# Optimization experiments

Hardware: AMD Instinct MI355X
Metric: run time of the kernel (lower is better)

Reference implementation:

```python
import jax, jax.numpy as jnp
import numpy as np

B, N, C, H = 8, 1024, 768, 12
HEAD_DIM = C // H
EPS = 1e-6


def setup_inputs() -> dict:
    key = jax.random.key(0)
    k1, k2, k3, k4, k5 = jax.random.split(key, 5)
    x = jax.random.normal(k1, (B, N, C), dtype=jnp.float32)
    # binary keep-mask per token, shape (B, N, 1)
    policy = (jax.random.uniform(k2, (B, N, 1)) > 0.3).astype(jnp.float32)
    Wqkv = jax.random.normal(k3, (3 * C, C), dtype=jnp.float32) * 0.02
    Wproj = jax.random.normal(k4, (C, C), dtype=jnp.float32) * 0.02
    bproj = jax.random.normal(k5, (C,), dtype=jnp.float32) * 0.02
    return {"x": x, "policy": policy, "Wqkv": Wqkv, "Wproj": Wproj, "bproj": bproj}


def softmax_with_policy(attn, policy, eps=EPS):
    # attn: (B,H,N,N), policy: (B,N,1) in {0,1}
    Bb, _, Nn, _ = attn.shape
    ap1 = policy.reshape(Bb, 1, 1, Nn)          # key mask
    ap2 = policy.reshape(Bb, 1, Nn, 1)          # query mask
    eye = jnp.eye(Nn, dtype=policy.dtype)[None, None]
    attn_policy = ap1 * ap2 + (1.0 - ap1) * eye  # (B,1,N,N)
    max_att = jnp.max(attn, axis=-1, keepdims=True)
    a = jnp.exp(attn - max_att).astype(jnp.float32) * attn_policy.astype(jnp.float32)
    a = (a + eps / Nn) / (jnp.sum(a, axis=-1, keepdims=True) + eps)
    return a.astype(attn.dtype)


def reference(x, policy, Wqkv, Wproj, bproj):
    Bb, Nn, Cc = x.shape
    scale = HEAD_DIM ** -0.5
    qkv = (x @ Wqkv.T).reshape(Bb, Nn, 3, H, HEAD_DIM).transpose(2, 0, 3, 1, 4)
    q, k, v = qkv[0], qkv[1], qkv[2]            # each (B,H,N,hd)
    attn = jnp.einsum('bhnd,bhmd->bhnm', q, k) * scale
    attn = softmax_with_policy(attn, policy)
    out = jnp.einsum('bhnm,bhmd->bhnd', attn, v)  # (B,H,N,hd)
    out = out.transpose(0, 2, 1, 3).reshape(Bb, Nn, Cc)
    return out @ Wproj.T + bproj
```

## Files before the change

kernel.cpp:

```cpp
#include <hip/hip_runtime.h>
#include <hip/hip_bf16.h>
#include <stdint.h>

#define Bdim 8
#define Nseq 1024
#define Cdim 768
#define Hn 12
#define HD 64
#define EPSf 1e-6f

typedef __bf16 bf16;
typedef __bf16 bf16x8 __attribute__((ext_vector_type(8)));
typedef float f32x4 __attribute__((ext_vector_type(4)));

static __device__ __forceinline__ void gload_lds16(const bf16* g, bf16* lds) {
  __builtin_amdgcn_global_load_lds(
      (const __attribute__((address_space(1))) uint32_t*)g,
      (__attribute__((address_space(3))) uint32_t*)lds, 16, 0, 0);
}

#define NX (Bdim * Nseq * Cdim)
#define NWQ (3 * Cdim * Cdim)
#define NWP (Cdim * Cdim)
__global__ __launch_bounds__(256) void cvt_all(
    const float* __restrict__ x, const float* __restrict__ wq, const float* __restrict__ wp,
    bf16* __restrict__ Xb, bf16* __restrict__ Wqb, bf16* __restrict__ Wpb,
    float* __restrict__ CS) {
  if (blockIdx.x < 24) CS[blockIdx.x * 256 + threadIdx.x] = 0.f;
  const int i = (blockIdx.x * 256 + threadIdx.x) * 8;
  const float* src;
  bf16* dst;
  int off;
  if (i < NX) { src = x; dst = Xb; off = i; }
  else if (i < NX + NWQ) { src = wq; dst = Wqb; off = i - NX; }
  else { src = wp; dst = Wpb; off = i - NX - NWQ; }
  float4 a = *(const float4*)(src + off);
  float4 b = *(const float4*)(src + off + 4);
  bf16x8 o;
  o[0] = (bf16)a.x; o[1] = (bf16)a.y; o[2] = (bf16)a.z; o[3] = (bf16)a.w;
  o[4] = (bf16)b.x; o[5] = (bf16)b.y; o[6] = (bf16)b.z; o[7] = (bf16)b.w;
  *(bf16x8*)(dst + off) = o;
}

__global__ __launch_bounds__(256) void gemm_qkv(
    const bf16* __restrict__ X, const bf16* __restrict__ W,
    bf16* __restrict__ Qb, bf16* __restrict__ Kb, bf16* __restrict__ Vt,
    float* __restrict__ CS) {
  __shared__ __align__(16) bf16 As[128 * 64];
  __shared__ __align__(16) bf16 Bs[128 * 64];
  const int t = threadIdx.x;
  const int lane = t & 63;
  const int w = t >> 6;
  const int l15 = lane & 15, quad = lane >> 4;
  const int wm = w & 1, wn = w >> 1;
  constexpr int K = Cdim;

  const int flat = blockIdx.y * 18 + blockIdx.x;
  const int xcd = flat & 7, idx = flat >> 3;
  const int my = (idx & 7) + xcd * 8;
  const int nx = idx >> 3;
  const int mbase = my * 128;
  const int nbase = nx * 128;

  const int srow = t >> 3, slot = t & 7;
  f32x4 acc[4][4] = {};

  for (int kt = 0; kt < K; kt += 64) {
#pragma unroll
    for (int j = 0; j < 4; j++) {
      const int row = j * 32 + srow;
      const int seg = slot ^ (row & 7);
      gload_lds16(X + (size_t)(mbase + row) * K + kt + seg * 8, As + (j * 256 + t) * 8);
    }
#pragma unroll
    for (int j = 0; j < 4; j++) {
      const int row = j * 32 + srow;
      const int seg = slot ^ (row & 7);
      gload_lds16(W + (size_t)(nbase + row) * K + kt + seg * 8, Bs + (j * 256 + t) * 8);
    }
    __syncthreads();
#pragma unroll
    for (int kh = 0; kh < 2; kh++) {
      bf16x8 a[4], b[4];
#pragma unroll
      for (int mt = 0; mt < 4; mt++) {
        const int row = wm * 64 + mt * 16 + l15;
        a[mt] = *(const bf16x8*)(As + row * 64 + ((kh * 4 + quad) ^ (row & 7)) * 8);
      }
#pragma unroll
      for (int nt = 0; nt < 4; nt++) {
        const int row = wn * 64 + nt * 16 + l15;
        b[nt] = *(const bf16x8*)(Bs + row * 64 + ((kh * 4 + quad) ^ (row & 7)) * 8);
      }
#pragma unroll
      for (int mt = 0; mt < 4; mt++)
#pragma unroll
        for (int nt = 0; nt < 4; nt++)
          acc[mt][nt] = __builtin_amdgcn_mfma_f32_16x16x32_bf16(a[mt], b[nt], acc[mt][nt], 0, 0, 0);
    }
    __syncthreads();
  }

  const int s = nbase / Cdim;
  const float oscale = (s == 0) ? 0.125f : 1.0f;
  const int jbase = (nbase % Cdim) + wn * 64;
  const int b0 = mbase >> 10;
#pragma unroll
  for (int nt = 0; nt < 4; nt++) {
    const int jj = jbase + nt * 16 + l15;
    const int h = jj >> 6, d = jj & 63;
#pragma unroll
    for (int mt = 0; mt < 4; mt++) {
#pragma unroll
      for (int r = 0; r < 4; r++) {
        const int m = mbase + wm * 64 + mt * 16 + quad * 4 + r;
        const int n = m & 1023;
        const bf16 v = (bf16)(acc[mt][nt][r] * oscale);
        const size_t bh = (size_t)b0 * Hn + h;
        if (s == 0)      Qb[(bh * Nseq + n) * HD + d] = v;
        else if (s == 1) Kb[(bh * Nseq + n) * HD + d] = v;
        else {
          const int nperm = (n & ~31) | (quad * 8 + (mt & 1) * 4 + r);
          Vt[(bh * HD + d) * Nseq + nperm] = v;
        }
      }
    }
  }
  if (s == 2) {
#pragma unroll
    for (int nt = 0; nt < 4; nt++) {
      float v = 0.f;
#pragma unroll
      for (int mt = 0; mt < 4; mt++)
#pragma unroll
        for (int r = 0; r < 4; r++) v += acc[mt][nt][r];
      v += __shfl_xor(v, 16);
      v += __shfl_xor(v, 32);
      if (quad == 0) {
        const int jj = jbase + nt * 16 + l15;
        atomicAdd(&CS[((size_t)b0 * Hn + (jj >> 6)) * HD + (jj & 63)], v);
      }
    }
  }
}

template <bool DIAG>
static __device__ __forceinline__ void smax_update(
    f32x4 (&S)[2][4], float (&mx)[2], float (&lrow)[2],
    const float (&polq)[2], const float4 (&pk)[4],
    int kt, int qbase, int quad, int l15) {
#pragma unroll
  for (int u = 0; u < 2; u++) {
    const float pm = polq[u];
    const int q = qbase + u * 16 + l15;
    float m4 = -1e30f, psum = 0.f;
#pragma unroll
    for (int kg = 0; kg < 4; kg++)
#pragma unroll
      for (int r = 0; r < 4; r++) m4 = fmaxf(m4, S[u][kg][r]);
    mx[u] = fmaxf(mx[u], m4);
#pragma unroll
    for (int kg = 0; kg < 4; kg++) {
      const float* pkk = (const float*)&pk[kg];
#pragma unroll
      for (int r = 0; r < 4; r++) {
        const float e = __expf(S[u][kg][r]);
        float p = e * (pkk[r] * pm);
        if (DIAG) p = (q == kt + kg * 16 + quad * 4 + r) ? e : p;
        S[u][kg][r] = p;
        psum += p;
      }
    }
    lrow[u] += psum;
  }
}

__global__ __launch_bounds__(256) void attn_fused(
    const bf16* __restrict__ Qb, const bf16* __restrict__ Kb, const bf16* __restrict__ Vt,
    const float* __restrict__ pol, const float* __restrict__ CS, bf16* __restrict__ O) {
  __shared__ __align__(16) bf16 Ks[2][64 * 64];
  __shared__ __align__(16) bf16 Vs[2][64 * 64];
  __shared__ float Ps[Nseq];
  const int t = threadIdx.x, w = t >> 6, lane = t & 63;
  const int l15 = lane & 15, quad = lane >> 4;

  const int bx = blockIdx.x;
  const int g = (bx & 7) + 8 * (bx >> 6);
  const int qt = (bx >> 3) & 7;
  const int b_ = g / Hn, h = g % Hn;
  const int qbase = qt * 128 + w * 32;
  const int ktdiag = qbase & ~63;

  const bf16* Qp = Qb + (size_t)g * Nseq * HD;
  const bf16* Kp = Kb + (size_t)g * Nseq * HD;
  const bf16* Vp = Vt + (size_t)g * HD * Nseq;
  const float* polb = pol + (size_t)b_ * Nseq;

  *(float4*)(Ps + t * 4) = *(const float4*)(polb + t * 4);

  const int ci0 = t, ci1 = t + 256;
  const int row0 = ci0 >> 3, seg0 = (ci0 & 7) ^ (row0 & 7);
  const int row1 = ci1 >> 3, seg1 = (ci1 & 7) ^ (row1 & 7);

  bf16x8 aq[2][2];
#pragma unroll
  for (int u = 0; u < 2; u++) {
    aq[u][0] = *(const bf16x8*)(Qp + (qbase + u * 16 + l15) * HD + quad * 8);
    aq[u][1] = *(const bf16x8*)(Qp + (qbase + u * 16 + l15) * HD + 32 + quad * 8);
  }
  float polq[2] = { polb[qbase + l15], polb[qbase + 16 + l15] };

  float mx[2] = { -1e30f, -1e30f }, lrow[2] = { 0.f, 0.f };
  f32x4 oacc[2][4] = {};

  gload_lds16(Kp + row0 * HD + seg0 * 8, &Ks[0][ci0 * 8]);
  gload_lds16(Kp + row1 * HD + seg1 * 8, &Ks[0][ci1 * 8]);
  gload_lds16(Vp + (size_t)row0 * Nseq + seg0 * 8, &Vs[0][ci0 * 8]);
  gload_lds16(Vp + (size_t)row1 * Nseq + seg1 * 8, &Vs[0][ci1 * 8]);

  for (int kt = 0; kt < Nseq; kt += 64) {
    const int buf = (kt >> 6) & 1;
    __syncthreads();
    if (kt + 64 < Nseq) {
      const int nb = buf ^ 1;
      gload_lds16(Kp + (kt + 64 + row0) * HD + seg0 * 8, &Ks[nb][ci0 * 8]);
      gload_lds16(Kp + (kt + 64 + row1) * HD + seg1 * 8, &Ks[nb][ci1 * 8]);
      gload_lds16(Vp + (size_t)row0 * Nseq + kt + 64 + seg0 * 8, &Vs[nb][ci0 * 8]);
      gload_lds16(Vp + (size_t)row1 * Nseq + kt + 64 + seg1 * 8, &Vs[nb][ci1 * 8]);
    }

    f32x4 S[2][4] = {};
#pragma unroll
    for (int kg = 0; kg < 4; kg++) {
      const int row = kg * 16 + l15;
      bf16x8 bk0 = *(const bf16x8*)(&Ks[buf][row * 64 + ((quad ^ (row & 7)) * 8)]);
      bf16x8 bk1 = *(const bf16x8*)(&Ks[buf][row * 64 + (((quad ^ 4) ^ (row & 7)) * 8)]);
#pragma unroll
      for (int u = 0; u < 2; u++) {
        S[u][kg] = __builtin_amdgcn_mfma_f32_16x16x32_bf16(bk0, aq[u][0], S[u][kg], 0, 0, 0);
        S[u][kg] = __builtin_amdgcn_mfma_f32_16x16x32_bf16(bk1, aq[u][1], S[u][kg], 0, 0, 0);
      }
    }

    float4 pk[4];
#pragma unroll
    for (int kg = 0; kg < 4; kg++)
      pk[kg] = *(const float4*)(Ps + kt + kg * 16 + quad * 4);

    if (kt == ktdiag)
      smax_update<true>(S, mx, lrow, polq, pk, kt, qbase, quad, l15);
    else
      smax_update<false>(S, mx, lrow, polq, pk, kt, qbase, quad, l15);

#pragma unroll
    for (int hh = 0; hh < 2; hh++) {
      bf16x8 ap[2];
#pragma unroll
      for (int u = 0; u < 2; u++)
#pragma unroll
        for (int j = 0; j < 4; j++) {
          ap[u][j] = (bf16)S[u][2 * hh][j];
          ap[u][4 + j] = (bf16)S[u][2 * hh + 1][j];
        }
#pragma unroll
      for (int c = 0; c < 4; c++) {
        const int row = c * 16 + l15;
        bf16x8 bv = *(const bf16x8*)(&Vs[buf][row * 64 + (((hh * 4 + quad) ^ (row & 7)) * 8)]);
#pragma unroll
        for (int u = 0; u < 2; u++)
          oacc[u][c] = __builtin_amdgcn_mfma_f32_16x16x32_bf16(ap[u], bv, oacc[u][c], 0, 0, 0);
      }
    }
  }

  const float epsN = EPSf / (float)Nseq;
  float rden[2][4], eterm[2][4];
#pragma unroll
  for (int u = 0; u < 2; u++) {
    float v = lrow[u];
    v += __shfl_xor(v, 16);
    v += __shfl_xor(v, 32);
    float m = mx[u];
    m = fmaxf(m, __shfl_xor(m, 16));
    m = fmaxf(m, __shfl_xor(m, 32));
    const float em = __expf(m);
    const float den = v + EPSf * em;
    const float eN = epsN * em;
    const int base = lane & 48;
#pragma unroll
    for (int r = 0; r < 4; r++) {
      rden[u][r] = 1.f / __shfl(den, base | (quad * 4 + r));
      eterm[u][r] = __shfl(eN, base | (quad * 4 + r));
    }
  }
  const float* CSp = CS + (size_t)g * HD;
#pragma unroll
  for (int c = 0; c < 4; c++) {
    const float cs = CSp[c * 16 + l15];
#pragma unroll
    for (int u = 0; u < 2; u++)
#pragma unroll
      for (int r = 0; r < 4; r++) {
        const int q = qbase + u * 16 + quad * 4 + r;
        const float val = (oacc[u][c][r] + cs * eterm[u][r]) * rden[u][r];
        O[((size_t)b_ * Nseq + q) * Cdim + h * 64 + c * 16 + l15] = (bf16)val;
      }
  }
}

__global__ __launch_bounds__(256) void gemm_proj(
    const bf16* __restrict__ A_, const bf16* __restrict__ W,
    const float* __restrict__ bias, float* __restrict__ out) {
  __shared__ __align__(16) bf16 As[64 * 64];
  __shared__ __align__(16) bf16 Bs[128 * 64];
  const int t = threadIdx.x;
  const int lane = t & 63;
  const int wn = t >> 6;
  const int l15 = lane & 15, quad = lane >> 4;
  constexpr int K = Cdim;

  const int flat = blockIdx.y * 6 + blockIdx.x;
  const int xcd = flat & 7, idx = flat >> 3;
  const int my = (idx & 15) + xcd * 16;
  const int nx = idx >> 4;
  const int mbase = my * 64;
  const int nbase = nx * 128;

  const int srow = t >> 3, slot = t & 7;
  f32x4 acc[4][2] = {};

  for (int kt = 0; kt < K; kt += 64) {
#pragma unroll
    for (int j = 0; j < 2; j++) {
      const int row = j * 32 + srow;
      const int seg = slot ^ (row & 7);
      gload_lds16(A_ + (size_t)(mbase + row) * K + kt + seg * 8, As + (j * 256 + t) * 8);
    }
#pragma unroll
    for (int j = 0; j < 4; j++) {
      const int row = j * 32 + srow;
      const int seg = slot ^ (row & 7);
      gload_lds16(W + (size_t)(nbase + row) * K + kt + seg * 8, Bs + (j * 256 + t) * 8);
    }
    __syncthreads();
#pragma unroll
    for (int kh = 0; kh < 2; kh++) {
      bf16x8 a[4], b[2];
#pragma unroll
      for (int mt = 0; mt < 4; mt++) {
        const int row = mt * 16 + l15;
        a[mt] = *(const bf16x8*)(As + row * 64 + ((kh * 4 + quad) ^ (row & 7)) * 8);
      }
#pragma unroll
      for (int nt = 0; nt < 2; nt++) {
        const int row = wn * 32 + nt * 16 + l15;
        b[nt] = *(const bf16x8*)(Bs + row * 64 + ((kh * 4 + quad) ^ (row & 7)) * 8);
      }
#pragma unroll
      for (int mt = 0; mt < 4; mt++)
#pragma unroll
        for (int nt = 0; nt < 2; nt++)
          acc[mt][nt] = __builtin_amdgcn_mfma_f32_16x16x32_bf16(a[mt], b[nt], acc[mt][nt], 0, 0, 0);
    }
    __syncthreads();
  }

#pragma unroll
  for (int nt = 0; nt < 2; nt++) {
    const int j = nbase + wn * 32 + nt * 16 + l15;
    const float bj = bias[j];
#pragma unroll
    for (int mt = 0; mt < 4; mt++)
#pragma unroll
      for (int r = 0; r < 4; r++) {
        const int m = mbase + mt * 16 + quad * 4 + r;
        out[(size_t)m * Cdim + j] = acc[mt][nt][r] + bj;
      }
  }
}

extern "C" void kernel_launch(void* const* d_in, const int* in_sizes, int n_in,
                              void* d_out, int out_size, void* d_ws, size_t ws_size,
                              hipStream_t stream) {
  const float* x = (const float*)d_in[0];
  const float* pol = (const float*)d_in[1];
  const float* Wqkv = (const float*)d_in[2];
  const float* Wproj = (const float*)d_in[3];
  const float* bproj = (const float*)d_in[4];
  float* out = (float*)d_out;
  char* ws = (char*)d_ws;

  const size_t SZ = (size_t)Bdim * Hn * Nseq * HD * sizeof(bf16);
  bf16* Qb = (bf16*)(ws);
  bf16* Kb = (bf16*)(ws + SZ);
  bf16* Vt = (bf16*)(ws + 2 * SZ);
  bf16* O  = (bf16*)(ws + 3 * SZ);
  float* CS = (float*)(ws + 4 * SZ);
  bf16* Xb = (bf16*)(ws + 4 * SZ + 32 * 1024);
  bf16* Wqkvb = Xb + (size_t)Bdim * Nseq * Cdim;
  bf16* Wprojb = Wqkvb + (size_t)3 * Cdim * Cdim;

  cvt_all<<<(NX + NWQ + NWP) / 2048, 256, 0, stream>>>(x, Wqkv, Wproj, Xb, Wqkvb, Wprojb, CS);
  gemm_qkv<<<dim3(18, 64), 256, 0, stream>>>(Xb, Wqkvb, Qb, Kb, Vt, CS);
  attn_fused<<<Bdim * Hn * (Nseq / 128), 256, 0, stream>>>(Qb, Kb, Vt, pol, CS, O);
  gemm_proj<<<dim3(6, 128), 256, 0, stream>>>(O, Wprojb, bproj, out);
}
```

Baseline: 212.5 us.

## Double-buffer LDS tiles with K-step 32 in QKV and projection GEMMs

Both GEMM kernels now use two LDS buffers holding 32-wide K slices instead of one 64-wide slice. The next slice is prefetched with global_load_lds while MFMAs run on the current one, and each iteration needs one barrier instead of two. The goal is to hide global-load latency behind compute. In exchange, the XOR swizzle is dropped, so the 64-byte row stride may cause LDS bank conflicts. There are also twice as many loop iterations and barriers.

```diff
diff --git a/kernel.cpp b/kernel.cpp
--- a/kernel.cpp
+++ b/kernel.cpp
@@ -46,8 +46,8 @@
     const bf16* __restrict__ X, const bf16* __restrict__ W,
     bf16* __restrict__ Qb, bf16* __restrict__ Kb, bf16* __restrict__ Vt,
     float* __restrict__ CS) {
-  __shared__ __align__(16) bf16 As[128 * 64];
-  __shared__ __align__(16) bf16 Bs[128 * 64];
+  __shared__ __align__(16) bf16 As[2][128 * 32];
+  __shared__ __align__(16) bf16 Bs[2][128 * 32];
   const int t = threadIdx.x;
   const int lane = t & 63;
   const int w = t >> 6;
@@ -62,43 +62,39 @@
   const int mbase = my * 128;
   const int nbase = nx * 128;
 
-  const int srow = t >> 3, slot = t & 7;
+  const int r0 = t >> 2, c0 = (t & 3) * 8;
+  const bf16* Ag = X + (size_t)(mbase + r0) * K + c0;
+  const bf16* Bg = W + (size_t)(nbase + r0) * K + c0;
+
   f32x4 acc[4][4] = {};
 
-  for (int kt = 0; kt < K; kt += 64) {
-#pragma unroll
-    for (int j = 0; j < 4; j++) {
-      const int row = j * 32 + srow;
-      const int seg = slot ^ (row & 7);
-      gload_lds16(X + (size_t)(mbase + row) * K + kt + seg * 8, As + (j * 256 + t) * 8);
-    }
-#pragma unroll
-    for (int j = 0; j < 4; j++) {
-      const int row = j * 32 + srow;
-      const int seg = slot ^ (row & 7);
-      gload_lds16(W + (size_t)(nbase + row) * K + kt + seg * 8, Bs + (j * 256 + t) * 8);
-    }
+  gload_lds16(Ag, &As[0][t * 8]);
+  gload_lds16(Ag + (size_t)64 * K, &As[0][2048 + t * 8]);
+  gload_lds16(Bg, &Bs[0][t * 8]);
+  gload_lds16(Bg + (size_t)64 * K, &Bs[0][2048 + t * 8]);
+
+  for (int kt = 0; kt < K; kt += 32) {
+    const int buf = (kt >> 5) & 1;
     __syncthreads();
-#pragma unroll
-    for (int kh = 0; kh < 2; kh++) {
-      bf16x8 a[4], b[4];
-#pragma unroll
-      for (int mt = 0; mt < 4; mt++) {
-        const int row = wm * 64 + mt * 16 + l15;
-        a[mt] = *(const bf16x8*)(As + row * 64 + ((kh * 4 + quad) ^ (row & 7)) * 8);
-      }
-#pragma unroll
-      for (int nt = 0; nt < 4; nt++) {
-        const int row = wn * 64 + nt * 16 + l15;
-        b[nt] = *(const bf16x8*)(Bs + row * 64 + ((kh * 4 + quad) ^ (row & 7)) * 8);
-      }
-#pragma unroll
-      for (int mt = 0; mt < 4; mt++)
-#pragma unroll
-        for (int nt = 0; nt < 4; nt++)
-          acc[mt][nt] = __builtin_amdgcn_mfma_f32_16x16x32_bf16(a[mt], b[nt], acc[mt][nt], 0, 0, 0);
-    }
-    __syncthreads();
+    if (kt + 32 < K) {
+      const int nb = buf ^ 1;
+      gload_lds16(Ag + kt + 32, &As[nb][t * 8]);
+      gload_lds16(Ag + (size_t)64 * K + kt + 32, &As[nb][2048 + t * 8]);
+      gload_lds16(Bg + kt + 32, &Bs[nb][t * 8]);
+      gload_lds16(Bg + (size_t)64 * K + kt + 32, &Bs[nb][2048 + t * 8]);
+    }
+    bf16x8 a[4], b[4];
+#pragma unroll
+    for (int mt = 0; mt < 4; mt++)
+      a[mt] = *(const bf16x8*)(&As[buf][(wm * 64 + mt * 16 + l15) * 32 + quad * 8]);
+#pragma unroll
+    for (int nt = 0; nt < 4; nt++)
+      b[nt] = *(const bf16x8*)(&Bs[buf][(wn * 64 + nt * 16 + l15) * 32 + quad * 8]);
+#pragma unroll
+    for (int mt = 0; mt < 4; mt++)
+#pragma unroll
+      for (int nt = 0; nt < 4; nt++)
+        acc[mt][nt] = __builtin_amdgcn_mfma_f32_16x16x32_bf16(a[mt], b[nt], acc[mt][nt], 0, 0, 0);
   }
 
   const int s = nbase / Cdim;
@@ -311,8 +307,8 @@
 __global__ __launch_bounds__(256) void gemm_proj(
     const bf16* __restrict__ A_, const bf16* __restrict__ W,
     const float* __restrict__ bias, float* __restrict__ out) {
-  __shared__ __align__(16) bf16 As[64 * 64];
-  __shared__ __align__(16) bf16 Bs[128 * 64];
+  __shared__ __align__(16) bf16 As[2][64 * 32];
+  __shared__ __align__(16) bf16 Bs[2][128 * 32];
   const int t = threadIdx.x;
   const int lane = t & 63;
   const int wn = t >> 6;
@@ -326,43 +322,37 @@
   const int mbase = my * 64;
   const int nbase = nx * 128;
 
-  const int srow = t >> 3, slot = t & 7;
+  const int r0 = t >> 2, c0 = (t & 3) * 8;
+  const bf16* Ag = A_ + (size_t)(mbase + r0) * K + c0;
+  const bf16* Bg = W + (size_t)(nbase + r0) * K + c0;
+
   f32x4 acc[4][2] = {};
 
-  for (int kt = 0; kt < K; kt += 64) {
-#pragma unroll
-    for (int j = 0; j < 2; j++) {
-      const int row = j * 32 + srow;
-      const int seg = slot ^ (row & 7);
-      gload_lds16(A_ + (size_t)(mbase + row) * K + kt + seg * 8, As + (j * 256 + t) * 8);
-    }
-#pragma unroll
-    for (int j = 0; j < 4; j++) {
-      const int row = j * 32 + srow;
-      const int seg = slot ^ (row & 7);
-      gload_lds16(W + (size_t)(nbase + row) * K + kt + seg * 8, Bs + (j * 256 + t) * 8);
-    }
+  gload_lds16(Ag, &As[0][t * 8]);
+  gload_lds16(Bg, &Bs[0][t * 8]);
+  gload_lds16(Bg + (size_t)64 * K, &Bs[0][2048 + t * 8]);
+
+  for (int kt = 0; kt < K; kt += 32) {
+    const int buf = (kt >> 5) & 1;
     __syncthreads();
-#pragma unroll
-    for (int kh = 0; kh < 2; kh++) {
-      bf16x8 a[4], b[2];
-#pragma unroll
-      for (int mt = 0; mt < 4; mt++) {
-        const int row = mt * 16 + l15;
-        a[mt] = *(const bf16x8*)(As + row * 64 + ((kh * 4 + quad) ^ (row & 7)) * 8);
-      }
-#pragma unroll
-      for (int nt = 0; nt < 2; nt++) {
-        const int row = wn * 32 + nt * 16 + l15;
-        b[nt] = *(const bf16x8*)(Bs + row * 64 + ((kh * 4 + quad) ^ (row & 7)) * 8);
-      }
-#pragma unroll
-      for (int mt = 0; mt < 4; mt++)
-#pragma unroll
-        for (int nt = 0; nt < 2; nt++)
-          acc[mt][nt] = __builtin_amdgcn_mfma_f32_16x16x32_bf16(a[mt], b[nt], acc[mt][nt], 0, 0, 0);
-    }
-    __syncthreads();
+    if (kt + 32 < K) {
+      const int nb = buf ^ 1;
+      gload_lds16(Ag + kt + 32, &As[nb][t * 8]);
+      gload_lds16(Bg + kt + 32, &Bs[nb][t * 8]);
+      gload_lds16(Bg + (size_t)64 * K + kt + 32, &Bs[nb][2048 + t * 8]);
+    }
+    bf16x8 a[4], b[2];
+#pragma unroll
+    for (int mt = 0; mt < 4; mt++)
+      a[mt] = *(const bf16x8*)(&As[buf][(mt * 16 + l15) * 32 + quad * 8]);
+#pragma unroll
+    for (int nt = 0; nt < 2; nt++)
+      b[nt] = *(const bf16x8*)(&Bs[buf][(wn * 32 + nt * 16 + l15) * 32 + quad * 8]);
+#pragma unroll
+    for (int mt = 0; mt < 4; mt++)
+#pragma unroll
+      for (int nt = 0; nt < 2; nt++)
+        acc[mt][nt] = __builtin_amdgcn_mfma_f32_16x16x32_bf16(a[mt], b[nt], acc[mt][nt], 0, 0, 0);
   }
 
 #pragma unroll
```

After: 214.1 us. Within noise of the previous version (+0.8%).

## Fuse x fp32-to-bf16 conversion into QKV GEMM and coalesce V transpose stores

Applied to the files above, without the earlier changes.

The QKV GEMM now loads fp32 x tiles straight into LDS and converts them to bf16 in registers. This drops the separate conversion pass over x and the bf16 copy written to the workspace, at the cost of a K-step halved to 32 and more LDS traffic per step. V-transpose output is staged through LDS so each thread writes 16-byte vectors instead of scattered scalar stores. The V column sums are written as per-block partials rather than atomics, and the attention kernel adds up 16 partials per element.

```diff
diff --git a/kernel.cpp b/kernel.cpp
--- a/kernel.cpp
+++ b/kernel.cpp
@@ -8,46 +8,47 @@
 #define Hn 12
 #define HD 64
 #define EPSf 1e-6f
+#define NCS (Bdim * Hn * HD)
 
 typedef __bf16 bf16;
 typedef __bf16 bf16x8 __attribute__((ext_vector_type(8)));
 typedef float f32x4 __attribute__((ext_vector_type(4)));
 
-static __device__ __forceinline__ void gload_lds16(const bf16* g, bf16* lds) {
+static __device__ __forceinline__ void gload_lds16(const void* g, void* lds) {
   __builtin_amdgcn_global_load_lds(
       (const __attribute__((address_space(1))) uint32_t*)g,
       (__attribute__((address_space(3))) uint32_t*)lds, 16, 0, 0);
 }
 
-#define NX (Bdim * Nseq * Cdim)
+static __device__ __forceinline__ bf16x8 cvt8(float4 a, float4 b) {
+  bf16x8 o;
+  o[0] = (bf16)a.x; o[1] = (bf16)a.y; o[2] = (bf16)a.z; o[3] = (bf16)a.w;
+  o[4] = (bf16)b.x; o[5] = (bf16)b.y; o[6] = (bf16)b.z; o[7] = (bf16)b.w;
+  return o;
+}
+
 #define NWQ (3 * Cdim * Cdim)
 #define NWP (Cdim * Cdim)
-__global__ __launch_bounds__(256) void cvt_all(
-    const float* __restrict__ x, const float* __restrict__ wq, const float* __restrict__ wp,
-    bf16* __restrict__ Xb, bf16* __restrict__ Wqb, bf16* __restrict__ Wpb,
-    float* __restrict__ CS) {
-  if (blockIdx.x < 24) CS[blockIdx.x * 256 + threadIdx.x] = 0.f;
+__global__ __launch_bounds__(256) void cvt_w(
+    const float* __restrict__ wq, const float* __restrict__ wp,
+    bf16* __restrict__ Wqb, bf16* __restrict__ Wpb) {
   const int i = (blockIdx.x * 256 + threadIdx.x) * 8;
   const float* src;
   bf16* dst;
   int off;
-  if (i < NX) { src = x; dst = Xb; off = i; }
-  else if (i < NX + NWQ) { src = wq; dst = Wqb; off = i - NX; }
-  else { src = wp; dst = Wpb; off = i - NX - NWQ; }
+  if (i < NWQ) { src = wq; dst = Wqb; off = i; }
+  else { src = wp; dst = Wpb; off = i - NWQ; }
   float4 a = *(const float4*)(src + off);
   float4 b = *(const float4*)(src + off + 4);
-  bf16x8 o;
-  o[0] = (bf16)a.x; o[1] = (bf16)a.y; o[2] = (bf16)a.z; o[3] = (bf16)a.w;
-  o[4] = (bf16)b.x; o[5] = (bf16)b.y; o[6] = (bf16)b.z; o[7] = (bf16)b.w;
-  *(bf16x8*)(dst + off) = o;
+  *(bf16x8*)(dst + off) = cvt8(a, b);
 }
 
 __global__ __launch_bounds__(256) void gemm_qkv(
-    const bf16* __restrict__ X, const bf16* __restrict__ W,
+    const float* __restrict__ X, const bf16* __restrict__ W,
     bf16* __restrict__ Qb, bf16* __restrict__ Kb, bf16* __restrict__ Vt,
     float* __restrict__ CS) {
-  __shared__ __align__(16) bf16 As[128 * 64];
-  __shared__ __align__(16) bf16 Bs[128 * 64];
+  __shared__ __align__(16) float As[128 * 32];
+  __shared__ __align__(16) bf16 Bsb[128 * 32];
   const int t = threadIdx.x;
   const int lane = t & 63;
   const int w = t >> 6;
@@ -62,71 +63,64 @@
   const int mbase = my * 128;
   const int nbase = nx * 128;
 
-  const int srow = t >> 3, slot = t & 7;
   f32x4 acc[4][4] = {};
 
-  for (int kt = 0; kt < K; kt += 64) {
+  for (int kt = 0; kt < K; kt += 32) {
 #pragma unroll
     for (int j = 0; j < 4; j++) {
-      const int row = j * 32 + srow;
-      const int seg = slot ^ (row & 7);
-      gload_lds16(X + (size_t)(mbase + row) * K + kt + seg * 8, As + (j * 256 + t) * 8);
-    }
-#pragma unroll
-    for (int j = 0; j < 4; j++) {
-      const int row = j * 32 + srow;
-      const int seg = slot ^ (row & 7);
-      gload_lds16(W + (size_t)(nbase + row) * K + kt + seg * 8, Bs + (j * 256 + t) * 8);
+      const int ci = j * 256 + t;
+      const int row = ci >> 3, seg = (ci & 7) ^ (row & 7);
+      gload_lds16(X + (size_t)(mbase + row) * K + kt + seg * 4, As + ci * 4);
+    }
+#pragma unroll
+    for (int j = 0; j < 2; j++) {
+      const int ci = j * 256 + t;
+      const int row = ci >> 2, seg = (ci & 3) ^ (row & 3);
+      gload_lds16(W + (size_t)(nbase + row) * K + kt + seg * 8, Bsb + ci * 8);
     }
     __syncthreads();
-#pragma unroll
-    for (int kh = 0; kh < 2; kh++) {
-      bf16x8 a[4], b[4];
-#pragma unroll
-      for (int mt = 0; mt < 4; mt++) {
-        const int row = wm * 64 + mt * 16 + l15;
-        a[mt] = *(const bf16x8*)(As + row * 64 + ((kh * 4 + quad) ^ (row & 7)) * 8);
-      }
-#pragma unroll
-      for (int nt = 0; nt < 4; nt++) {
-        const int row = wn * 64 + nt * 16 + l15;
-        b[nt] = *(const bf16x8*)(Bs + row * 64 + ((kh * 4 + quad) ^ (row & 7)) * 8);
-      }
-#pragma unroll
-      for (int mt = 0; mt < 4; mt++)
-#pragma unroll
-        for (int nt = 0; nt < 4; nt++)
-          acc[mt][nt] = __builtin_amdgcn_mfma_f32_16x16x32_bf16(a[mt], b[nt], acc[mt][nt], 0, 0, 0);
-    }
+    bf16x8 a[4], b[4];
+#pragma unroll
+    for (int mt = 0; mt < 4; mt++) {
+      const int row = wm * 64 + mt * 16 + l15;
+      float4 f0 = *(const float4*)&As[row * 32 + ((2 * quad) ^ (row & 7)) * 4];
+      float4 f1 = *(const float4*)&As[row * 32 + ((2 * quad + 1) ^ (row & 7)) * 4];
+      a[mt] = cvt8(f0, f1);
+    }
+#pragma unroll
+    for (int nt = 0; nt < 4; nt++) {
+      const int row = wn * 64 + nt * 16 + l15;
+      b[nt] = *(const bf16x8*)&Bsb[row * 32 + (quad ^ (row & 3)) * 8];
+    }
+#pragma unroll
+    for (int mt = 0; mt < 4; mt++)
+#pragma unroll
+      for (int nt = 0; nt < 4; nt++)
+        acc[mt][nt] = __builtin_amdgcn_mfma_f32_16x16x32_bf16(a[mt], b[nt], acc[mt][nt], 0, 0, 0);
     __syncthreads();
   }
 
   const int s = nbase / Cdim;
-  const float oscale = (s == 0) ? 0.125f : 1.0f;
   const int jbase = (nbase % Cdim) + wn * 64;
   const int b0 = mbase >> 10;
-#pragma unroll
-  for (int nt = 0; nt < 4; nt++) {
-    const int jj = jbase + nt * 16 + l15;
-    const int h = jj >> 6, d = jj & 63;
-#pragma unroll
-    for (int mt = 0; mt < 4; mt++) {
-#pragma unroll
-      for (int r = 0; r < 4; r++) {
-        const int m = mbase + wm * 64 + mt * 16 + quad * 4 + r;
-        const int n = m & 1023;
-        const bf16 v = (bf16)(acc[mt][nt][r] * oscale);
-        const size_t bh = (size_t)b0 * Hn + h;
-        if (s == 0)      Qb[(bh * Nseq + n) * HD + d] = v;
-        else if (s == 1) Kb[(bh * Nseq + n) * HD + d] = v;
-        else {
-          const int nperm = (n & ~31) | (quad * 8 + (mt & 1) * 4 + r);
-          Vt[(bh * HD + d) * Nseq + nperm] = v;
+
+  if (s < 2) {
+    const float oscale = (s == 0) ? 0.125f : 1.0f;
+    bf16* Out = (s == 0) ? Qb : Kb;
+#pragma unroll
+    for (int nt = 0; nt < 4; nt++) {
+      const int jj = jbase + nt * 16 + l15;
+      const int h = jj >> 6, d = jj & 63;
+#pragma unroll
+      for (int mt = 0; mt < 4; mt++)
+#pragma unroll
+        for (int r = 0; r < 4; r++) {
+          const int m = mbase + wm * 64 + mt * 16 + quad * 4 + r;
+          Out[(((size_t)b0 * Hn + h) * Nseq + (m & 1023)) * HD + d] =
+              (bf16)(acc[mt][nt][r] * oscale);
         }
-      }
-    }
-  }
-  if (s == 2) {
+    }
+  } else {
 #pragma unroll
     for (int nt = 0; nt < 4; nt++) {
       float v = 0.f;
@@ -138,8 +132,37 @@
       v += __shfl_xor(v, 32);
       if (quad == 0) {
         const int jj = jbase + nt * 16 + l15;
-        atomicAdd(&CS[((size_t)b0 * Hn + (jj >> 6)) * HD + (jj & 63)], v);
-      }
+        CS[((my & 7) * 2 + wm) * NCS + ((size_t)b0 * Hn + (jj >> 6)) * HD + (jj & 63)] = v;
+      }
+    }
+    bf16* T = (bf16*)As;
+    const int jb0 = nbase - 2 * Cdim;
+    const int nb0 = mbase & 1023;
+    const int c32s = t >> 3, n0 = (t & 7) * 16;
+#pragma unroll
+    for (int p = 0; p < 4; p++) {
+      __syncthreads();
+      if (wn == (p >> 1)) {
+#pragma unroll
+        for (int q2 = 0; q2 < 2; q2++) {
+          const int nt = (p & 1) * 2 + q2;
+          const int c32 = q2 * 16 + l15;
+#pragma unroll
+          for (int mt = 0; mt < 4; mt++)
+#pragma unroll
+            for (int r = 0; r < 4; r++) {
+              const int Lp = wm * 64 + (mt >> 1) * 32 + quad * 8 + (mt & 1) * 4 + r;
+              T[c32 * 136 + Lp] = (bf16)acc[mt][nt][r];
+            }
+        }
+      }
+      __syncthreads();
+      const int jj = jb0 + p * 32 + c32s;
+      bf16x8 v0 = *(const bf16x8*)&T[c32s * 136 + n0];
+      bf16x8 v1 = *(const bf16x8*)&T[c32s * 136 + n0 + 8];
+      bf16* dst = Vt + (((size_t)b0 * Hn + (jj >> 6)) * HD + (jj & 63)) * Nseq + nb0 + n0;
+      *(bf16x8*)dst = v0;
+      *(bf16x8*)(dst + 8) = v1;
     }
   }
 }
@@ -293,10 +316,12 @@
       eterm[u][r] = __shfl(eN, base | (quad * 4 + r));
     }
   }
-  const float* CSp = CS + (size_t)g * HD;
+  const float* CSg = CS + (size_t)g * HD;
 #pragma unroll
   for (int c = 0; c < 4; c++) {
-    const float cs = CSp[c * 16 + l15];
+    float cs = 0.f;
+#pragma unroll
+    for (int p2 = 0; p2 < 16; p2++) cs += CSg[p2 * NCS + c * 16 + l15];
 #pragma unroll
     for (int u = 0; u < 2; u++)
 #pragma unroll
@@ -396,12 +421,11 @@
   bf16* Vt = (bf16*)(ws + 2 * SZ);
   bf16* O  = (bf16*)(ws + 3 * SZ);
   float* CS = (float*)(ws + 4 * SZ);
-  bf16* Xb = (bf16*)(ws + 4 * SZ + 32 * 1024);
-  bf16* Wqkvb = Xb + (size_t)Bdim * Nseq * Cdim;
-  bf16* Wprojb = Wqkvb + (size_t)3 * Cdim * Cdim;
-
-  cvt_all<<<(NX + NWQ + NWP) / 2048, 256, 0, stream>>>(x, Wqkv, Wproj, Xb, Wqkvb, Wprojb, CS);
-  gemm_qkv<<<dim3(18, 64), 256, 0, stream>>>(Xb, Wqkvb, Qb, Kb, Vt, CS);
+  bf16* Wqkvb = (bf16*)(ws + 4 * SZ + 16 * NCS * 4);
+  bf16* Wprojb = Wqkvb + (size_t)NWQ;
+
+  cvt_w<<<(NWQ + NWP) / 2048, 256, 0, stream>>>(Wqkv, Wproj, Wqkvb, Wprojb);
+  gemm_qkv<<<dim3(18, 64), 256, 0, stream>>>(x, Wqkvb, Qb, Kb, Vt, CS);
   attn_fused<<<Bdim * Hn * (Nseq / 128), 256, 0, stream>>>(Qb, Kb, Vt, pol, CS, O);
   gemm_proj<<<dim3(6, 128), 256, 0, stream>>>(O, Wprojb, bproj, out);
 }
```

New measurement: 217.3 us. +2.2%, slower.
